# Kernel optimization log

Hardware: AMD Instinct MI355X
Metric: run time of the kernel (lower is better)

Reference implementation:

```python
import jax, jax.numpy as jnp
import numpy as np

ALPHA = 1.0
LORA_DIM = 4
MULTIPLIER = 1.0


def setup_inputs() -> dict:
    key = jax.random.key(0)
    ks = jax.random.split(key, 6)
    B, S, IN, OUT = 4, 4096, 4096, 4096
    x = jax.random.normal(ks[0], (B, S, IN), dtype=jnp.float32)
    W0 = jax.random.normal(ks[1], (OUT, IN), dtype=jnp.float32) * 0.02
    b = jax.random.normal(ks[2], (OUT,), dtype=jnp.float32) * 0.02
    # factorization(4096) -> (64, 64) for both in and out dims
    lokr_w1 = jax.random.normal(ks[3], (64, 64), dtype=jnp.float32) * 0.1
    lokr_w2_a = jax.random.normal(ks[4], (64, LORA_DIM), dtype=jnp.float32) * 0.1
    lokr_w2_b = jax.random.normal(ks[5], (LORA_DIM, 64), dtype=jnp.float32) * 0.1
    return {"x": x, "W0": W0, "b": b, "lokr_w1": lokr_w1,
            "lokr_w2_a": lokr_w2_a, "lokr_w2_b": lokr_w2_b}


def reference(x, W0, b, lokr_w1, lokr_w2_a, lokr_w2_b):
    # Original (frozen) linear forward
    result = jnp.einsum('bsi,oi->bso', x, W0) + b
    # LoKr delta weight: kron(w1, w2_a @ w2_b) * (alpha / lora_dim) * multiplier
    w2 = lokr_w2_a @ lokr_w2_b                      # (out_k, in_n) = (64, 64)
    scale = ALPHA / LORA_DIM
    diff_weight = jnp.kron(lokr_w1, w2) * (scale * MULTIPLIER)  # (4096, 4096)
    delta = jnp.einsum('bsi,oi->bso', x, diff_weight)
    return result + delta
```

## Files before the change

### kernel.cpp

```cpp
#include <hip/hip_runtime.h>
#include <hip/hip_bf16.h>
#include <stdint.h>

#define M_DIM 16384
#define N_DIM 4096
#define K_DIM 4096
#define NT    (K_DIM / 64)

typedef float f32x4 __attribute__((ext_vector_type(4)));
typedef short bf16x8 __attribute__((ext_vector_type(8)));
typedef unsigned short u16;

__device__ __forceinline__ unsigned short f32_to_bf16(float f) {
    union { float f; uint32_t u; } v; v.f = f;
    uint32_t u = v.u;
    uint32_t r = (u + 0x7FFFu + ((u >> 16) & 1u)) >> 16;
    return (unsigned short)r;
}

__device__ __forceinline__ void gload16(const void* g, void* l) {
    __builtin_amdgcn_global_load_lds(
        (const __attribute__((address_space(1))) void*)g,
        (__attribute__((address_space(3))) void*)l,
        16, 0, 0);
}

__global__ void build_weff(const float* __restrict__ W0,
                           const float* __restrict__ w1,
                           const float* __restrict__ w2a,
                           const float* __restrict__ w2b,
                           u16* __restrict__ Weff) {
    long idx = (long)blockIdx.x * 256 + threadIdx.x;
    long e0 = idx * 4;
    int o  = (int)(e0 >> 12);
    int i0 = (int)(e0 & 4095);
    int r  = o & 63;
    float a0 = w2a[r * 4 + 0], a1 = w2a[r * 4 + 1];
    float a2 = w2a[r * 4 + 2], a3 = w2a[r * 4 + 3];
    float w1v = w1[(o >> 6) * 64 + (i0 >> 6)] * 0.25f;
    float4 w0 = *(const float4*)(W0 + e0);
    const float* w0p = (const float*)&w0;
    unsigned short outp[4];
#pragma unroll
    for (int j = 0; j < 4; ++j) {
        int c = (i0 + j) & 63;
        float w2 = a0 * w2b[0 * 64 + c] + a1 * w2b[1 * 64 + c]
                 + a2 * w2b[2 * 64 + c] + a3 * w2b[3 * 64 + c];
        outp[j] = f32_to_bf16(w0p[j] + w1v * w2);
    }
    *(ushort4*)(Weff + e0) = make_ushort4(outp[0], outp[1], outp[2], outp[3]);
}

__global__ void cvt_x(const float* __restrict__ x, u16* __restrict__ xb) {
    long idx = (long)blockIdx.x * 256 + threadIdx.x;
    long e0 = idx * 8;
    float4 v0 = *(const float4*)(x + e0);
    float4 v1 = *(const float4*)(x + e0 + 4);
    union { unsigned short s[8]; int4 v; } o;
    const float* p0 = (const float*)&v0;
    const float* p1 = (const float*)&v1;
#pragma unroll
    for (int j = 0; j < 4; ++j) o.s[j]     = f32_to_bf16(p0[j]);
#pragma unroll
    for (int j = 0; j < 4; ++j) o.s[4 + j] = f32_to_bf16(p1[j]);
    *(int4*)(xb + e0) = o.v;
}

__global__ __launch_bounds__(512, 2) void gemm_8p(
        const u16* __restrict__ A,
        const u16* __restrict__ Bm,
        const float* __restrict__ bias,
        float* __restrict__ C) {
    __shared__ __align__(16) u16 ldsA[2][2][8192];
    __shared__ __align__(16) u16 ldsB[2][2][8192];

    const int tid = threadIdx.x;
    const int bid = blockIdx.x;
    const int swz = (bid & 7) * 128 + (bid >> 3);
    const int tm = swz >> 4;
    const int tn = swz & 15;
    const int mBase = tm * 256;
    const int nBase = tn * 256;

    const int lane = tid & 63;
    const int wave = tid >> 6;
    const int wr = wave >> 2;
    const int wc = wave & 3;

    const int srow = tid >> 2;
    const int slog = (tid & 3) ^ ((srow >> 1) & 3);
    const u16* aS0 = A  + (size_t)(mBase + srow)       * K_DIM + slog * 8;
    const u16* aS1 = A  + (size_t)(mBase + srow + 128) * K_DIM + slog * 8;
    const u16* bS0 = Bm + (size_t)(nBase + srow)       * K_DIM + slog * 8;
    const u16* bS1 = Bm + (size_t)(nBase + srow + 128) * K_DIM + slog * 8;

#define STAGE_A(buf, t, ks) do { const size_t _k = (size_t)(t) * 64 + (ks) * 32; \
        gload16(aS0 + _k, &ldsA[buf][ks][tid * 8]);                              \
        gload16(aS1 + _k, &ldsA[buf][ks][4096 + tid * 8]); } while (0)
#define STAGE_B(buf, t, ks) do { const size_t _k = (size_t)(t) * 64 + (ks) * 32; \
        gload16(bS0 + _k, &ldsB[buf][ks][tid * 8]);                              \
        gload16(bS1 + _k, &ldsB[buf][ks][4096 + tid * 8]); } while (0)

    const int rl = lane & 15, cbk = lane >> 4;
    const int sslot = cbk ^ ((rl >> 1) & 3);
    const int aRd = (wr * 128 + rl) * 32 + sslot * 8;
    const int bRd = (wc * 64  + rl) * 32 + sslot * 8;

#define RD_A(buf, ks, m) (*(const bf16x8*)&ldsA[buf][ks][aRd + (m) * 512])
#define RD_B(buf, ks, n) (*(const bf16x8*)&ldsB[buf][ks][bRd + (n) * 512])

    f32x4 acc[8][4] = {};
    bf16x8 va0, va1, va2, va3, vb0, vb1, vb2, vb3;

#define MFMA_ROW(mh)                                                                  \
    acc[(mh)*4+0][0] = __builtin_amdgcn_mfma_f32_16x16x32_bf16(va0, vb0, acc[(mh)*4+0][0], 0, 0, 0); \
    acc[(mh)*4+0][1] = __builtin_amdgcn_mfma_f32_16x16x32_bf16(va0, vb1, acc[(mh)*4+0][1], 0, 0, 0); \
    acc[(mh)*4+0][2] = __builtin_amdgcn_mfma_f32_16x16x32_bf16(va0, vb2, acc[(mh)*4+0][2], 0, 0, 0); \
    acc[(mh)*4+0][3] = __builtin_amdgcn_mfma_f32_16x16x32_bf16(va0, vb3, acc[(mh)*4+0][3], 0, 0, 0); \
    acc[(mh)*4+1][0] = __builtin_amdgcn_mfma_f32_16x16x32_bf16(va1, vb0, acc[(mh)*4+1][0], 0, 0, 0); \
    acc[(mh)*4+1][1] = __builtin_amdgcn_mfma_f32_16x16x32_bf16(va1, vb1, acc[(mh)*4+1][1], 0, 0, 0); \
    acc[(mh)*4+1][2] = __builtin_amdgcn_mfma_f32_16x16x32_bf16(va1, vb2, acc[(mh)*4+1][2], 0, 0, 0); \
    acc[(mh)*4+1][3] = __builtin_amdgcn_mfma_f32_16x16x32_bf16(va1, vb3, acc[(mh)*4+1][3], 0, 0, 0); \
    acc[(mh)*4+2][0] = __builtin_amdgcn_mfma_f32_16x16x32_bf16(va2, vb0, acc[(mh)*4+2][0], 0, 0, 0); \
    acc[(mh)*4+2][1] = __builtin_amdgcn_mfma_f32_16x16x32_bf16(va2, vb1, acc[(mh)*4+2][1], 0, 0, 0); \
    acc[(mh)*4+2][2] = __builtin_amdgcn_mfma_f32_16x16x32_bf16(va2, vb2, acc[(mh)*4+2][2], 0, 0, 0); \
    acc[(mh)*4+2][3] = __builtin_amdgcn_mfma_f32_16x16x32_bf16(va2, vb3, acc[(mh)*4+2][3], 0, 0, 0); \
    acc[(mh)*4+3][0] = __builtin_amdgcn_mfma_f32_16x16x32_bf16(va3, vb0, acc[(mh)*4+3][0], 0, 0, 0); \
    acc[(mh)*4+3][1] = __builtin_amdgcn_mfma_f32_16x16x32_bf16(va3, vb1, acc[(mh)*4+3][1], 0, 0, 0); \
    acc[(mh)*4+3][2] = __builtin_amdgcn_mfma_f32_16x16x32_bf16(va3, vb2, acc[(mh)*4+3][2], 0, 0, 0); \
    acc[(mh)*4+3][3] = __builtin_amdgcn_mfma_f32_16x16x32_bf16(va3, vb3, acc[(mh)*4+3][3], 0, 0, 0);

#define PHASE0(buf, ks, VM, ...) do {                                   \
        __builtin_amdgcn_s_barrier();                                   \
        va0 = RD_A(buf, ks, 0);                                         \
        vb0 = RD_B(buf, ks, 0); vb1 = RD_B(buf, ks, 1);                 \
        vb2 = RD_B(buf, ks, 2); vb3 = RD_B(buf, ks, 3);                 \
        va1 = RD_A(buf, ks, 1); va2 = RD_A(buf, ks, 2);                 \
        va3 = RD_A(buf, ks, 3);                                         \
        __VA_ARGS__;                                                    \
        __builtin_amdgcn_s_setprio(1);                                  \
        MFMA_ROW(0)                                                     \
        __builtin_amdgcn_s_setprio(0);                                  \
        __builtin_amdgcn_sched_barrier(0);                              \
        if (VM) asm volatile("s_waitcnt vmcnt(6)" ::: "memory");        \
    } while (0)
#define PHASE1(buf, ks, VM, ...) do {                                   \
        __builtin_amdgcn_s_barrier();                                   \
        va0 = RD_A(buf, ks, 4); va1 = RD_A(buf, ks, 5);                 \
        va2 = RD_A(buf, ks, 6); va3 = RD_A(buf, ks, 7);                 \
        __VA_ARGS__;                                                    \
        __builtin_amdgcn_s_setprio(1);                                  \
        MFMA_ROW(1)                                                     \
        __builtin_amdgcn_s_setprio(0);                                  \
        __builtin_amdgcn_sched_barrier(0);                              \
        if (VM) asm volatile("s_waitcnt vmcnt(6)" ::: "memory");        \
    } while (0)

    STAGE_B(0, 0, 0); STAGE_A(0, 0, 0); STAGE_B(0, 0, 1); STAGE_A(0, 0, 1);
    asm volatile("s_waitcnt vmcnt(4)" ::: "memory");
    STAGE_B(1, 1, 0); STAGE_A(1, 1, 0); STAGE_B(1, 1, 1);
    asm volatile("s_waitcnt vmcnt(6)" ::: "memory");

    for (int it = 0; it < NT / 2; ++it) {
        const int t1 = 2 * it + 1;
        const int t2 = (2 * it + 2 < NT) ? 2 * it + 2 : NT - 1;
        const int t3 = (2 * it + 3 < NT) ? 2 * it + 3 : NT - 1;
        PHASE0(0, 0, 0, STAGE_A(1, t1, 1));
        PHASE1(0, 0, 0, STAGE_B(0, t2, 0));
        PHASE0(0, 1, 0, STAGE_A(0, t2, 0));
        PHASE1(0, 1, 1, STAGE_B(0, t2, 1));
        PHASE0(1, 0, 0, STAGE_A(0, t2, 1));
        PHASE1(1, 0, 0, STAGE_B(1, t3, 0));
        PHASE0(1, 1, 0, STAGE_A(1, t3, 0));
        PHASE1(1, 1, 1, STAGE_B(1, t3, 1));
    }
    asm volatile("s_waitcnt vmcnt(0)" ::: "memory");

#pragma unroll
    for (int n = 0; n < 4; ++n) {
        const int col = nBase + wc * 64 + n * 16 + rl;
        const float bv = bias[col];
#pragma unroll
        for (int m = 0; m < 8; ++m) {
            const int row = mBase + wr * 128 + m * 16 + cbk * 4;
#pragma unroll
            for (int j = 0; j < 4; ++j)
                C[(size_t)(row + j) * N_DIM + col] = acc[m][n][j] + bv;
        }
    }
#undef STAGE_A
#undef STAGE_B
#undef RD_A
#undef RD_B
#undef MFMA_ROW
#undef PHASE0
#undef PHASE1
}

__global__ void naive_fallback(const float* __restrict__ x,
                               const float* __restrict__ W0,
                               const float* __restrict__ b,
                               const float* __restrict__ w1,
                               const float* __restrict__ w2a,
                               const float* __restrict__ w2b,
                               float* __restrict__ out) {
    __shared__ float w2s[64 * 64];
    for (int t = threadIdx.x; t < 4096; t += blockDim.x) {
        int rr = t >> 6, cc = t & 63;
        float s = 0.f;
        for (int k = 0; k < 4; ++k) s += w2a[rr * 4 + k] * w2b[k * 64 + cc];
        w2s[t] = s * 0.25f;
    }
    __syncthreads();
    long idx = (long)blockIdx.x * blockDim.x + threadIdx.x;
    int m = (int)(idx >> 12);
    int o = (int)(idx & 4095);
    const float* xr = x + (long)m * K_DIM;
    const float* wrp = W0 + (long)o * K_DIM;
    int ob = (o >> 6) * 64, orr = (o & 63) * 64;
    float acc = 0.f;
    for (int i = 0; i < K_DIM; ++i) {
        float w = wrp[i] + w1[ob + (i >> 6)] * w2s[orr + (i & 63)];
        acc += xr[i] * w;
    }
    out[idx] = acc + b[o];
}

extern "C" void kernel_launch(void* const* d_in, const int* in_sizes, int n_in,
                              void* d_out, int out_size, void* d_ws, size_t ws_size,
                              hipStream_t stream) {
    const float* x   = (const float*)d_in[0];
    const float* W0  = (const float*)d_in[1];
    const float* b   = (const float*)d_in[2];
    const float* w1  = (const float*)d_in[3];
    const float* w2a = (const float*)d_in[4];
    const float* w2b = (const float*)d_in[5];
    float* out = (float*)d_out;

    const size_t xb_bytes = (size_t)M_DIM * K_DIM * 2;
    const size_t wf_bytes = (size_t)N_DIM * K_DIM * 2;

    if (ws_size >= xb_bytes + wf_bytes) {
        u16* xb = (u16*)d_ws;
        u16* wf = (u16*)((char*)d_ws + xb_bytes);
        build_weff<<<(N_DIM * (long)K_DIM) / 4 / 256, 256, 0, stream>>>(W0, w1, w2a, w2b, wf);
        cvt_x<<<((long)M_DIM * K_DIM) / 8 / 256, 256, 0, stream>>>(x, xb);
        gemm_8p<<<(M_DIM / 256) * (N_DIM / 256), 512, 0, stream>>>(xb, wf, b, out);
    } else {
        naive_fallback<<<((long)M_DIM * N_DIM) / 256, 256, 0, stream>>>(
            x, W0, b, w1, w2a, w2b, out);
    }
}
```

Measured before the change: 625.9 us.

## Software-pipeline LDS fragment reads one phase ahead of MFMA compute

```diff
diff --git a/kernel.cpp b/kernel.cpp
--- a/kernel.cpp
+++ b/kernel.cpp
@@ -110,71 +110,117 @@
 #define RD_B(buf, ks, n) (*(const bf16x8*)&ldsB[buf][ks][bRd + (n) * 512])
 
     f32x4 acc[8][4] = {};
-    bf16x8 va0, va1, va2, va3, vb0, vb1, vb2, vb3;
-
-#define MFMA_ROW(mh)                                                                  \
-    acc[(mh)*4+0][0] = __builtin_amdgcn_mfma_f32_16x16x32_bf16(va0, vb0, acc[(mh)*4+0][0], 0, 0, 0); \
-    acc[(mh)*4+0][1] = __builtin_amdgcn_mfma_f32_16x16x32_bf16(va0, vb1, acc[(mh)*4+0][1], 0, 0, 0); \
-    acc[(mh)*4+0][2] = __builtin_amdgcn_mfma_f32_16x16x32_bf16(va0, vb2, acc[(mh)*4+0][2], 0, 0, 0); \
-    acc[(mh)*4+0][3] = __builtin_amdgcn_mfma_f32_16x16x32_bf16(va0, vb3, acc[(mh)*4+0][3], 0, 0, 0); \
-    acc[(mh)*4+1][0] = __builtin_amdgcn_mfma_f32_16x16x32_bf16(va1, vb0, acc[(mh)*4+1][0], 0, 0, 0); \
-    acc[(mh)*4+1][1] = __builtin_amdgcn_mfma_f32_16x16x32_bf16(va1, vb1, acc[(mh)*4+1][1], 0, 0, 0); \
-    acc[(mh)*4+1][2] = __builtin_amdgcn_mfma_f32_16x16x32_bf16(va1, vb2, acc[(mh)*4+1][2], 0, 0, 0); \
-    acc[(mh)*4+1][3] = __builtin_amdgcn_mfma_f32_16x16x32_bf16(va1, vb3, acc[(mh)*4+1][3], 0, 0, 0); \
-    acc[(mh)*4+2][0] = __builtin_amdgcn_mfma_f32_16x16x32_bf16(va2, vb0, acc[(mh)*4+2][0], 0, 0, 0); \
-    acc[(mh)*4+2][1] = __builtin_amdgcn_mfma_f32_16x16x32_bf16(va2, vb1, acc[(mh)*4+2][1], 0, 0, 0); \
-    acc[(mh)*4+2][2] = __builtin_amdgcn_mfma_f32_16x16x32_bf16(va2, vb2, acc[(mh)*4+2][2], 0, 0, 0); \
-    acc[(mh)*4+2][3] = __builtin_amdgcn_mfma_f32_16x16x32_bf16(va2, vb3, acc[(mh)*4+2][3], 0, 0, 0); \
-    acc[(mh)*4+3][0] = __builtin_amdgcn_mfma_f32_16x16x32_bf16(va3, vb0, acc[(mh)*4+3][0], 0, 0, 0); \
-    acc[(mh)*4+3][1] = __builtin_amdgcn_mfma_f32_16x16x32_bf16(va3, vb1, acc[(mh)*4+3][1], 0, 0, 0); \
-    acc[(mh)*4+3][2] = __builtin_amdgcn_mfma_f32_16x16x32_bf16(va3, vb2, acc[(mh)*4+3][2], 0, 0, 0); \
-    acc[(mh)*4+3][3] = __builtin_amdgcn_mfma_f32_16x16x32_bf16(va3, vb3, acc[(mh)*4+3][3], 0, 0, 0);
-
-#define PHASE0(buf, ks, VM, ...) do {                                   \
-        __builtin_amdgcn_s_barrier();                                   \
-        va0 = RD_A(buf, ks, 0);                                         \
-        vb0 = RD_B(buf, ks, 0); vb1 = RD_B(buf, ks, 1);                 \
-        vb2 = RD_B(buf, ks, 2); vb3 = RD_B(buf, ks, 3);                 \
-        va1 = RD_A(buf, ks, 1); va2 = RD_A(buf, ks, 2);                 \
-        va3 = RD_A(buf, ks, 3);                                         \
-        __VA_ARGS__;                                                    \
-        __builtin_amdgcn_s_setprio(1);                                  \
-        MFMA_ROW(0)                                                     \
-        __builtin_amdgcn_s_setprio(0);                                  \
-        __builtin_amdgcn_sched_barrier(0);                              \
-        if (VM) asm volatile("s_waitcnt vmcnt(6)" ::: "memory");        \
-    } while (0)
-#define PHASE1(buf, ks, VM, ...) do {                                   \
-        __builtin_amdgcn_s_barrier();                                   \
-        va0 = RD_A(buf, ks, 4); va1 = RD_A(buf, ks, 5);                 \
-        va2 = RD_A(buf, ks, 6); va3 = RD_A(buf, ks, 7);                 \
-        __VA_ARGS__;                                                    \
-        __builtin_amdgcn_s_setprio(1);                                  \
-        MFMA_ROW(1)                                                     \
-        __builtin_amdgcn_s_setprio(0);                                  \
-        __builtin_amdgcn_sched_barrier(0);                              \
-        if (VM) asm volatile("s_waitcnt vmcnt(6)" ::: "memory");        \
-    } while (0)
+    bf16x8 aA0, aA1, aA2, aA3;
+    bf16x8 aB0, aB1, aB2, aB3;
+    bf16x8 bX0, bX1, bX2, bX3;
+    bf16x8 bY0, bY1, bY2, bY3;
+
+#define MFMA16(A0_,A1_,A2_,A3_,B0_,B1_,B2_,B3_,mh)                                      \
+    acc[(mh)*4+0][0] = __builtin_amdgcn_mfma_f32_16x16x32_bf16(A0_, B0_, acc[(mh)*4+0][0], 0, 0, 0); \
+    acc[(mh)*4+0][1] = __builtin_amdgcn_mfma_f32_16x16x32_bf16(A0_, B1_, acc[(mh)*4+0][1], 0, 0, 0); \
+    acc[(mh)*4+0][2] = __builtin_amdgcn_mfma_f32_16x16x32_bf16(A0_, B2_, acc[(mh)*4+0][2], 0, 0, 0); \
+    acc[(mh)*4+0][3] = __builtin_amdgcn_mfma_f32_16x16x32_bf16(A0_, B3_, acc[(mh)*4+0][3], 0, 0, 0); \
+    acc[(mh)*4+1][0] = __builtin_amdgcn_mfma_f32_16x16x32_bf16(A1_, B0_, acc[(mh)*4+1][0], 0, 0, 0); \
+    acc[(mh)*4+1][1] = __builtin_amdgcn_mfma_f32_16x16x32_bf16(A1_, B1_, acc[(mh)*4+1][1], 0, 0, 0); \
+    acc[(mh)*4+1][2] = __builtin_amdgcn_mfma_f32_16x16x32_bf16(A1_, B2_, acc[(mh)*4+1][2], 0, 0, 0); \
+    acc[(mh)*4+1][3] = __builtin_amdgcn_mfma_f32_16x16x32_bf16(A1_, B3_, acc[(mh)*4+1][3], 0, 0, 0); \
+    acc[(mh)*4+2][0] = __builtin_amdgcn_mfma_f32_16x16x32_bf16(A2_, B0_, acc[(mh)*4+2][0], 0, 0, 0); \
+    acc[(mh)*4+2][1] = __builtin_amdgcn_mfma_f32_16x16x32_bf16(A2_, B1_, acc[(mh)*4+2][1], 0, 0, 0); \
+    acc[(mh)*4+2][2] = __builtin_amdgcn_mfma_f32_16x16x32_bf16(A2_, B2_, acc[(mh)*4+2][2], 0, 0, 0); \
+    acc[(mh)*4+2][3] = __builtin_amdgcn_mfma_f32_16x16x32_bf16(A2_, B3_, acc[(mh)*4+2][3], 0, 0, 0); \
+    acc[(mh)*4+3][0] = __builtin_amdgcn_mfma_f32_16x16x32_bf16(A3_, B0_, acc[(mh)*4+3][0], 0, 0, 0); \
+    acc[(mh)*4+3][1] = __builtin_amdgcn_mfma_f32_16x16x32_bf16(A3_, B1_, acc[(mh)*4+3][1], 0, 0, 0); \
+    acc[(mh)*4+3][2] = __builtin_amdgcn_mfma_f32_16x16x32_bf16(A3_, B2_, acc[(mh)*4+3][2], 0, 0, 0); \
+    acc[(mh)*4+3][3] = __builtin_amdgcn_mfma_f32_16x16x32_bf16(A3_, B3_, acc[(mh)*4+3][3], 0, 0, 0);
+
+#define RD_BSET(set, buf, ks)                                   \
+    set##0 = RD_B(buf, ks, 0); set##1 = RD_B(buf, ks, 1);       \
+    set##2 = RD_B(buf, ks, 2); set##3 = RD_B(buf, ks, 3);
+#define RD_ALO(buf, ks)                                         \
+    aA0 = RD_A(buf, ks, 0); aA1 = RD_A(buf, ks, 1);             \
+    aA2 = RD_A(buf, ks, 2); aA3 = RD_A(buf, ks, 3);
+#define RD_AHI(buf, ks)                                         \
+    aB0 = RD_A(buf, ks, 4); aB1 = RD_A(buf, ks, 5);             \
+    aB2 = RD_A(buf, ks, 6); aB3 = RD_A(buf, ks, 7);
+
+#define PH_END() do { __builtin_amdgcn_sched_barrier(0);        \
+                      __builtin_amdgcn_s_barrier(); } while (0)
 
     STAGE_B(0, 0, 0); STAGE_A(0, 0, 0); STAGE_B(0, 0, 1); STAGE_A(0, 0, 1);
-    asm volatile("s_waitcnt vmcnt(4)" ::: "memory");
     STAGE_B(1, 1, 0); STAGE_A(1, 1, 0); STAGE_B(1, 1, 1);
     asm volatile("s_waitcnt vmcnt(6)" ::: "memory");
+    __builtin_amdgcn_s_barrier();
+    RD_BSET(bX, 0, 0)
+    RD_ALO(0, 0)
 
     for (int it = 0; it < NT / 2; ++it) {
         const int t1 = 2 * it + 1;
         const int t2 = (2 * it + 2 < NT) ? 2 * it + 2 : NT - 1;
         const int t3 = (2 * it + 3 < NT) ? 2 * it + 3 : NT - 1;
-        PHASE0(0, 0, 0, STAGE_A(1, t1, 1));
-        PHASE1(0, 0, 0, STAGE_B(0, t2, 0));
-        PHASE0(0, 1, 0, STAGE_A(0, t2, 0));
-        PHASE1(0, 1, 1, STAGE_B(0, t2, 1));
-        PHASE0(1, 0, 0, STAGE_A(0, t2, 1));
-        PHASE1(1, 0, 0, STAGE_B(1, t3, 0));
-        PHASE0(1, 1, 0, STAGE_A(1, t3, 0));
-        PHASE1(1, 1, 1, STAGE_B(1, t3, 1));
-    }
-    asm volatile("s_waitcnt vmcnt(0)" ::: "memory");
+
+        STAGE_A(1, t1, 1);
+        RD_AHI(0, 0)
+        __builtin_amdgcn_s_setprio(1);
+        MFMA16(aA0, aA1, aA2, aA3, bX0, bX1, bX2, bX3, 0)
+        __builtin_amdgcn_s_setprio(0);
+        PH_END();
+
+        STAGE_B(0, t2, 0);
+        RD_BSET(bY, 0, 1)
+        RD_ALO(0, 1)
+        __builtin_amdgcn_s_setprio(1);
+        MFMA16(aB0, aB1, aB2, aB3, bX0, bX1, bX2, bX3, 1)
+        __builtin_amdgcn_s_setprio(0);
+        PH_END();
+
+        STAGE_A(0, t2, 0);
+        RD_AHI(0, 1)
+        __builtin_amdgcn_s_setprio(1);
+        MFMA16(aA0, aA1, aA2, aA3, bY0, bY1, bY2, bY3, 0)
+        __builtin_amdgcn_s_setprio(0);
+        asm volatile("s_waitcnt vmcnt(4)" ::: "memory");
+        PH_END();
+
+        STAGE_B(0, t2, 1);
+        RD_BSET(bX, 1, 0)
+        RD_ALO(1, 0)
+        __builtin_amdgcn_s_setprio(1);
+        MFMA16(aB0, aB1, aB2, aB3, bY0, bY1, bY2, bY3, 1)
+        __builtin_amdgcn_s_setprio(0);
+        PH_END();
+
+        STAGE_A(0, t2, 1);
+        RD_AHI(1, 0)
+        __builtin_amdgcn_s_setprio(1);
+        MFMA16(aA0, aA1, aA2, aA3, bX0, bX1, bX2, bX3, 0)
+        __builtin_amdgcn_s_setprio(0);
+        PH_END();
+
+        STAGE_B(1, t3, 0);
+        RD_BSET(bY, 1, 1)
+        RD_ALO(1, 1)
+        __builtin_amdgcn_s_setprio(1);
+        MFMA16(aB0, aB1, aB2, aB3, bX0, bX1, bX2, bX3, 1)
+        __builtin_amdgcn_s_setprio(0);
+        PH_END();
+
+        STAGE_A(1, t3, 0);
+        RD_AHI(1, 1)
+        __builtin_amdgcn_s_setprio(1);
+        MFMA16(aA0, aA1, aA2, aA3, bY0, bY1, bY2, bY3, 0)
+        __builtin_amdgcn_s_setprio(0);
+        asm volatile("s_waitcnt vmcnt(4)" ::: "memory");
+        PH_END();
+
+        STAGE_B(1, t3, 1);
+        RD_BSET(bX, 0, 0)
+        RD_ALO(0, 0)
+        __builtin_amdgcn_s_setprio(1);
+        MFMA16(aB0, aB1, aB2, aB3, bY0, bY1, bY2, bY3, 1)
+        __builtin_amdgcn_s_setprio(0);
+        PH_END();
+    }
+    asm volatile("s_waitcnt vmcnt(0) lgkmcnt(0)" ::: "memory");
 
 #pragma unroll
     for (int n = 0; n < 4; ++n) {
@@ -192,9 +238,11 @@
 #undef STAGE_B
 #undef RD_A
 #undef RD_B
-#undef MFMA_ROW
-#undef PHASE0
-#undef PHASE1
+#undef RD_BSET
+#undef RD_ALO
+#undef RD_AHI
+#undef MFMA16
+#undef PH_END
 }
 
 __global__ void naive_fallback(const float* __restrict__ x,
```

Result: slower. 647.9 us (+3.5%).

## Switch GEMM to 32x32x16 MFMA tiles and merge prep kernels

Applied to the files above, without the earlier changes.

```diff
diff --git a/kernel.cpp b/kernel.cpp
--- a/kernel.cpp
+++ b/kernel.cpp
@@ -7,7 +7,8 @@
 #define K_DIM 4096
 #define NT    (K_DIM / 64)
 
-typedef float f32x4 __attribute__((ext_vector_type(4)));
+typedef float f32x4  __attribute__((ext_vector_type(4)));
+typedef float f32x16 __attribute__((ext_vector_type(16)));
 typedef short bf16x8 __attribute__((ext_vector_type(8)));
 typedef unsigned short u16;
 
@@ -25,45 +26,48 @@
         16, 0, 0);
 }
 
-__global__ void build_weff(const float* __restrict__ W0,
-                           const float* __restrict__ w1,
-                           const float* __restrict__ w2a,
-                           const float* __restrict__ w2b,
-                           u16* __restrict__ Weff) {
-    long idx = (long)blockIdx.x * 256 + threadIdx.x;
-    long e0 = idx * 4;
-    int o  = (int)(e0 >> 12);
-    int i0 = (int)(e0 & 4095);
-    int r  = o & 63;
-    float a0 = w2a[r * 4 + 0], a1 = w2a[r * 4 + 1];
-    float a2 = w2a[r * 4 + 2], a3 = w2a[r * 4 + 3];
-    float w1v = w1[(o >> 6) * 64 + (i0 >> 6)] * 0.25f;
-    float4 w0 = *(const float4*)(W0 + e0);
-    const float* w0p = (const float*)&w0;
-    unsigned short outp[4];
+__global__ void prep(const float* __restrict__ W0,
+                     const float* __restrict__ w1,
+                     const float* __restrict__ w2a,
+                     const float* __restrict__ w2b,
+                     const float* __restrict__ x,
+                     u16* __restrict__ Weff,
+                     u16* __restrict__ xb) {
+    const int bid = blockIdx.x;
+    if (bid < 16384) {
+        long idx = (long)bid * 256 + threadIdx.x;
+        long e0 = idx * 4;
+        int o  = (int)(e0 >> 12);
+        int i0 = (int)(e0 & 4095);
+        int r  = o & 63;
+        float a0 = w2a[r * 4 + 0], a1 = w2a[r * 4 + 1];
+        float a2 = w2a[r * 4 + 2], a3 = w2a[r * 4 + 3];
+        float w1v = w1[(o >> 6) * 64 + (i0 >> 6)] * 0.25f;
+        float4 w0 = *(const float4*)(W0 + e0);
+        const float* w0p = (const float*)&w0;
+        unsigned short outp[4];
 #pragma unroll
-    for (int j = 0; j < 4; ++j) {
-        int c = (i0 + j) & 63;
-        float w2 = a0 * w2b[0 * 64 + c] + a1 * w2b[1 * 64 + c]
-                 + a2 * w2b[2 * 64 + c] + a3 * w2b[3 * 64 + c];
-        outp[j] = f32_to_bf16(w0p[j] + w1v * w2);
-    }
-    *(ushort4*)(Weff + e0) = make_ushort4(outp[0], outp[1], outp[2], outp[3]);
-}
-
-__global__ void cvt_x(const float* __restrict__ x, u16* __restrict__ xb) {
-    long idx = (long)blockIdx.x * 256 + threadIdx.x;
-    long e0 = idx * 8;
-    float4 v0 = *(const float4*)(x + e0);
-    float4 v1 = *(const float4*)(x + e0 + 4);
-    union { unsigned short s[8]; int4 v; } o;
-    const float* p0 = (const float*)&v0;
-    const float* p1 = (const float*)&v1;
+        for (int j = 0; j < 4; ++j) {
+            int c = (i0 + j) & 63;
+            float w2 = a0 * w2b[0 * 64 + c] + a1 * w2b[1 * 64 + c]
+                     + a2 * w2b[2 * 64 + c] + a3 * w2b[3 * 64 + c];
+            outp[j] = f32_to_bf16(w0p[j] + w1v * w2);
+        }
+        *(ushort4*)(Weff + e0) = make_ushort4(outp[0], outp[1], outp[2], outp[3]);
+    } else {
+        long idx = (long)(bid - 16384) * 256 + threadIdx.x;
+        long e0 = idx * 8;
+        float4 v0 = *(const float4*)(x + e0);
+        float4 v1 = *(const float4*)(x + e0 + 4);
+        union { unsigned short s[8]; int4 v; } o;
+        const float* p0 = (const float*)&v0;
+        const float* p1 = (const float*)&v1;
 #pragma unroll
-    for (int j = 0; j < 4; ++j) o.s[j]     = f32_to_bf16(p0[j]);
+        for (int j = 0; j < 4; ++j) o.s[j]     = f32_to_bf16(p0[j]);
 #pragma unroll
-    for (int j = 0; j < 4; ++j) o.s[4 + j] = f32_to_bf16(p1[j]);
-    *(int4*)(xb + e0) = o.v;
+        for (int j = 0; j < 4; ++j) o.s[4 + j] = f32_to_bf16(p1[j]);
+        *(int4*)(xb + e0) = o.v;
+    }
 }
 
 __global__ __launch_bounds__(512, 2) void gemm_8p(
@@ -101,100 +105,98 @@
         gload16(bS0 + _k, &ldsB[buf][ks][tid * 8]);                              \
         gload16(bS1 + _k, &ldsB[buf][ks][4096 + tid * 8]); } while (0)
 
-    const int rl = lane & 15, cbk = lane >> 4;
-    const int sslot = cbk ^ ((rl >> 1) & 3);
-    const int aRd = (wr * 128 + rl) * 32 + sslot * 8;
-    const int bRd = (wc * 64  + rl) * 32 + sslot * 8;
-
-#define RD_A(buf, ks, m) (*(const bf16x8*)&ldsA[buf][ks][aRd + (m) * 512])
-#define RD_B(buf, ks, n) (*(const bf16x8*)&ldsB[buf][ks][bRd + (n) * 512])
-
-    f32x4 acc[8][4] = {};
-    bf16x8 va0, va1, va2, va3, vb0, vb1, vb2, vb3;
-
-#define MFMA_ROW(mh)                                                                  \
-    acc[(mh)*4+0][0] = __builtin_amdgcn_mfma_f32_16x16x32_bf16(va0, vb0, acc[(mh)*4+0][0], 0, 0, 0); \
-    acc[(mh)*4+0][1] = __builtin_amdgcn_mfma_f32_16x16x32_bf16(va0, vb1, acc[(mh)*4+0][1], 0, 0, 0); \
-    acc[(mh)*4+0][2] = __builtin_amdgcn_mfma_f32_16x16x32_bf16(va0, vb2, acc[(mh)*4+0][2], 0, 0, 0); \
-    acc[(mh)*4+0][3] = __builtin_amdgcn_mfma_f32_16x16x32_bf16(va0, vb3, acc[(mh)*4+0][3], 0, 0, 0); \
-    acc[(mh)*4+1][0] = __builtin_amdgcn_mfma_f32_16x16x32_bf16(va1, vb0, acc[(mh)*4+1][0], 0, 0, 0); \
-    acc[(mh)*4+1][1] = __builtin_amdgcn_mfma_f32_16x16x32_bf16(va1, vb1, acc[(mh)*4+1][1], 0, 0, 0); \
-    acc[(mh)*4+1][2] = __builtin_amdgcn_mfma_f32_16x16x32_bf16(va1, vb2, acc[(mh)*4+1][2], 0, 0, 0); \
-    acc[(mh)*4+1][3] = __builtin_amdgcn_mfma_f32_16x16x32_bf16(va1, vb3, acc[(mh)*4+1][3], 0, 0, 0); \
-    acc[(mh)*4+2][0] = __builtin_amdgcn_mfma_f32_16x16x32_bf16(va2, vb0, acc[(mh)*4+2][0], 0, 0, 0); \
-    acc[(mh)*4+2][1] = __builtin_amdgcn_mfma_f32_16x16x32_bf16(va2, vb1, acc[(mh)*4+2][1], 0, 0, 0); \
-    acc[(mh)*4+2][2] = __builtin_amdgcn_mfma_f32_16x16x32_bf16(va2, vb2, acc[(mh)*4+2][2], 0, 0, 0); \
-    acc[(mh)*4+2][3] = __builtin_amdgcn_mfma_f32_16x16x32_bf16(va2, vb3, acc[(mh)*4+2][3], 0, 0, 0); \
-    acc[(mh)*4+3][0] = __builtin_amdgcn_mfma_f32_16x16x32_bf16(va3, vb0, acc[(mh)*4+3][0], 0, 0, 0); \
-    acc[(mh)*4+3][1] = __builtin_amdgcn_mfma_f32_16x16x32_bf16(va3, vb1, acc[(mh)*4+3][1], 0, 0, 0); \
-    acc[(mh)*4+3][2] = __builtin_amdgcn_mfma_f32_16x16x32_bf16(va3, vb2, acc[(mh)*4+3][2], 0, 0, 0); \
-    acc[(mh)*4+3][3] = __builtin_amdgcn_mfma_f32_16x16x32_bf16(va3, vb3, acc[(mh)*4+3][3], 0, 0, 0);
-
-#define PHASE0(buf, ks, VM, ...) do {                                   \
+    const int rl32 = lane & 31, g = lane >> 5;
+    const int rowA0 = wr * 128 + rl32;
+    const int rowB0 = wc * 64 + rl32;
+    const int swA = (rowA0 >> 1) & 3;
+    const int swB = (rowB0 >> 1) & 3;
+    const int aBase = rowA0 * 32;
+    const int bBase = rowB0 * 32;
+    const int sa0 = ((0 + g) ^ swA) * 8, sa1 = ((2 + g) ^ swA) * 8;
+    const int sb0 = ((0 + g) ^ swB) * 8, sb1 = ((2 + g) ^ swB) * 8;
+
+#define RD_A(buf, ks, mi, sk) (*(const bf16x8*)&ldsA[buf][ks][aBase + (mi) * 1024 + (sk)])
+#define RD_B(buf, ks, nh, sk) (*(const bf16x8*)&ldsB[buf][ks][bBase + (nh) * 1024 + (sk)])
+
+    f32x16 acc00 = {}, acc01 = {}, acc10 = {}, acc11 = {};
+    f32x16 acc20 = {}, acc21 = {}, acc30 = {}, acc31 = {};
+    bf16x8 a00, a01, a10, a11, a20, a21, a30, a31;
+    bf16x8 b0, b1;
+
+#define MFMA8(AC0, AC1, AC2, AC3)                                              \
+    AC0 = __builtin_amdgcn_mfma_f32_32x32x16_bf16(a00, b0, AC0, 0, 0, 0);      \
+    AC1 = __builtin_amdgcn_mfma_f32_32x32x16_bf16(a10, b0, AC1, 0, 0, 0);      \
+    AC2 = __builtin_amdgcn_mfma_f32_32x32x16_bf16(a20, b0, AC2, 0, 0, 0);      \
+    AC3 = __builtin_amdgcn_mfma_f32_32x32x16_bf16(a30, b0, AC3, 0, 0, 0);      \
+    AC0 = __builtin_amdgcn_mfma_f32_32x32x16_bf16(a01, b1, AC0, 0, 0, 0);      \
+    AC1 = __builtin_amdgcn_mfma_f32_32x32x16_bf16(a11, b1, AC1, 0, 0, 0);      \
+    AC2 = __builtin_amdgcn_mfma_f32_32x32x16_bf16(a21, b1, AC2, 0, 0, 0);      \
+    AC3 = __builtin_amdgcn_mfma_f32_32x32x16_bf16(a31, b1, AC3, 0, 0, 0);
+
+#define PH_N0(buf, ks, ...) do {                                        \
         __builtin_amdgcn_s_barrier();                                   \
-        va0 = RD_A(buf, ks, 0);                                         \
-        vb0 = RD_B(buf, ks, 0); vb1 = RD_B(buf, ks, 1);                 \
-        vb2 = RD_B(buf, ks, 2); vb3 = RD_B(buf, ks, 3);                 \
-        va1 = RD_A(buf, ks, 1); va2 = RD_A(buf, ks, 2);                 \
-        va3 = RD_A(buf, ks, 3);                                         \
+        b0  = RD_B(buf, ks, 0, sb0); b1  = RD_B(buf, ks, 0, sb1);       \
+        a00 = RD_A(buf, ks, 0, sa0); a01 = RD_A(buf, ks, 0, sa1);       \
+        a10 = RD_A(buf, ks, 1, sa0); a11 = RD_A(buf, ks, 1, sa1);       \
+        a20 = RD_A(buf, ks, 2, sa0); a21 = RD_A(buf, ks, 2, sa1);       \
+        a30 = RD_A(buf, ks, 3, sa0); a31 = RD_A(buf, ks, 3, sa1);       \
         __VA_ARGS__;                                                    \
         __builtin_amdgcn_s_setprio(1);                                  \
-        MFMA_ROW(0)                                                     \
+        MFMA8(acc00, acc10, acc20, acc30)                               \
         __builtin_amdgcn_s_setprio(0);                                  \
         __builtin_amdgcn_sched_barrier(0);                              \
-        if (VM) asm volatile("s_waitcnt vmcnt(6)" ::: "memory");        \
     } while (0)
-#define PHASE1(buf, ks, VM, ...) do {                                   \
+#define PH_N1(buf, ks) do {                                             \
         __builtin_amdgcn_s_barrier();                                   \
-        va0 = RD_A(buf, ks, 4); va1 = RD_A(buf, ks, 5);                 \
-        va2 = RD_A(buf, ks, 6); va3 = RD_A(buf, ks, 7);                 \
-        __VA_ARGS__;                                                    \
+        b0  = RD_B(buf, ks, 1, sb0); b1  = RD_B(buf, ks, 1, sb1);       \
         __builtin_amdgcn_s_setprio(1);                                  \
-        MFMA_ROW(1)                                                     \
+        MFMA8(acc01, acc11, acc21, acc31)                               \
         __builtin_amdgcn_s_setprio(0);                                  \
         __builtin_amdgcn_sched_barrier(0);                              \
-        if (VM) asm volatile("s_waitcnt vmcnt(6)" ::: "memory");        \
+        asm volatile("s_waitcnt vmcnt(8)" ::: "memory");                \
     } while (0)
 
     STAGE_B(0, 0, 0); STAGE_A(0, 0, 0); STAGE_B(0, 0, 1); STAGE_A(0, 0, 1);
+    STAGE_B(1, 1, 0); STAGE_A(1, 1, 0);
     asm volatile("s_waitcnt vmcnt(4)" ::: "memory");
-    STAGE_B(1, 1, 0); STAGE_A(1, 1, 0); STAGE_B(1, 1, 1);
-    asm volatile("s_waitcnt vmcnt(6)" ::: "memory");
 
     for (int it = 0; it < NT / 2; ++it) {
         const int t1 = 2 * it + 1;
         const int t2 = (2 * it + 2 < NT) ? 2 * it + 2 : NT - 1;
         const int t3 = (2 * it + 3 < NT) ? 2 * it + 3 : NT - 1;
-        PHASE0(0, 0, 0, STAGE_A(1, t1, 1));
-        PHASE1(0, 0, 0, STAGE_B(0, t2, 0));
-        PHASE0(0, 1, 0, STAGE_A(0, t2, 0));
-        PHASE1(0, 1, 1, STAGE_B(0, t2, 1));
-        PHASE0(1, 0, 0, STAGE_A(0, t2, 1));
-        PHASE1(1, 0, 0, STAGE_B(1, t3, 0));
-        PHASE0(1, 1, 0, STAGE_A(1, t3, 0));
-        PHASE1(1, 1, 1, STAGE_B(1, t3, 1));
-    }
-    asm volatile("s_waitcnt vmcnt(0)" ::: "memory");
-
-#pragma unroll
-    for (int n = 0; n < 4; ++n) {
-        const int col = nBase + wc * 64 + n * 16 + rl;
-        const float bv = bias[col];
-#pragma unroll
-        for (int m = 0; m < 8; ++m) {
-            const int row = mBase + wr * 128 + m * 16 + cbk * 4;
-#pragma unroll
-            for (int j = 0; j < 4; ++j)
-                C[(size_t)(row + j) * N_DIM + col] = acc[m][n][j] + bv;
-        }
-    }
+        PH_N0(0, 0, STAGE_B(1, t1, 1); STAGE_A(1, t1, 1));
+        PH_N1(0, 0);
+        PH_N0(0, 1, STAGE_B(0, t2, 0); STAGE_A(0, t2, 0));
+        PH_N1(0, 1);
+        PH_N0(1, 0, STAGE_B(0, t2, 1); STAGE_A(0, t2, 1));
+        PH_N1(1, 0);
+        PH_N0(1, 1, STAGE_B(1, t3, 0); STAGE_A(1, t3, 0));
+        PH_N1(1, 1);
+    }
+    asm volatile("s_waitcnt vmcnt(0) lgkmcnt(0)" ::: "memory");
+
+#define STORE_T(ACC, mi, nh) do {                                              \
+        const int col = nBase + wc * 64 + (nh) * 32 + rl32;                    \
+        const float bv = bias[col];                                            \
+        _Pragma("unroll")                                                      \
+        for (int r = 0; r < 16; ++r) {                                         \
+            const int row = mBase + wr * 128 + (mi) * 32 +                     \
+                            (r & 3) + 8 * (r >> 2) + 4 * g;                    \
+            C[(size_t)row * N_DIM + col] = ACC[r] + bv;                        \
+        }                                                                      \
+    } while (0)
+    STORE_T(acc00, 0, 0); STORE_T(acc01, 0, 1);
+    STORE_T(acc10, 1, 0); STORE_T(acc11, 1, 1);
+    STORE_T(acc20, 2, 0); STORE_T(acc21, 2, 1);
+    STORE_T(acc30, 3, 0); STORE_T(acc31, 3, 1);
 #undef STAGE_A
 #undef STAGE_B
 #undef RD_A
 #undef RD_B
-#undef MFMA_ROW
-#undef PHASE0
-#undef PHASE1
+#undef MFMA8
+#undef PH_N0
+#undef PH_N1
+#undef STORE_T
 }
 
 __global__ void naive_fallback(const float* __restrict__ x,
@@ -243,8 +245,7 @@
     if (ws_size >= xb_bytes + wf_bytes) {
         u16* xb = (u16*)d_ws;
         u16* wf = (u16*)((char*)d_ws + xb_bytes);
-        build_weff<<<(N_DIM * (long)K_DIM) / 4 / 256, 256, 0, stream>>>(W0, w1, w2a, w2b, wf);
-        cvt_x<<<((long)M_DIM * K_DIM) / 8 / 256, 256, 0, stream>>>(x, xb);
+        prep<<<49152, 256, 0, stream>>>(W0, w1, w2a, w2b, x, wf, xb);
         gemm_8p<<<(M_DIM / 256) * (N_DIM / 256), 512, 0, stream>>>(xb, wf, b, out);
     } else {
         naive_fallback<<<((long)M_DIM * N_DIM) / 256, 256, 0, stream>>>(
```

Result: slower. 676.5 us (+8.1%).
